# Kernel tuning notes

Hardware: AMD Instinct MI355X
Metric: run time of the kernel (lower is better)

Reference implementation:

```python
import jax, jax.numpy as jnp
import numpy as np

N = 20000      # nodes
E = 320000     # edges
IN = 128       # in_channels
HID = 64       # hidden_channels (per-head out dim, concat=False -> mean over heads)
HEADS = 4
NEG_SLOPE = 0.2


def setup_inputs() -> dict:
    key = jax.random.key(0)
    ks = jax.random.split(key, 18)
    g = lambda i, shape: jax.random.normal(ks[i], shape, dtype=jnp.float32) * 0.05
    return {
        "x": jax.random.normal(ks[0], (N, IN), dtype=jnp.float32),
        "edge_index": jax.random.randint(ks[1], (2, E), 0, N),
        # GATConv params: lin weight (no bias in PyG lin), att_src/att_dst, out bias
        "W0": g(2, (IN, HEADS * HID)),
        "W1": g(3, (HID, HEADS * HID)),
        "W2": g(4, (HID, HEADS * HID)),
        "W3": g(5, (HID, HEADS * HID)),
        "a_src": g(6, (4, HEADS, HID)),
        "a_dst": g(7, (4, HEADS, HID)),
        "gat_b": g(8, (4, HID)),
        # residual projection for layer 0 (in_channels != hidden_channels)
        "res_W": g(9, (IN, HID)),
        "res_b": g(10, (HID,)),
        # edge classifier MLP: 2*HID -> HID -> HID -> 1
        "lin_W0": g(11, (2 * HID, HID)),
        "lin_b0": g(12, (HID,)),
        "lin_W1": g(13, (HID, HID)),
        "lin_b1": g(14, (HID,)),
        "lin_W2": g(15, (HID, 1)),
        "lin_b2": g(16, (1,)),
    }


def gat_conv(x, src, dst, W, asrc, adst, b, n):
    # x: [n, F_in]; src/dst: [E_tot] (self-loops included); W: [F_in, H*C]
    h = (x @ W).reshape(n, HEADS, HID)                     # [n, H, C]
    s_src = (h * asrc).sum(-1)                             # [n, H]
    s_dst = (h * adst).sum(-1)                             # [n, H]
    e = jax.nn.leaky_relu(s_src[src] + s_dst[dst], NEG_SLOPE)  # [E_tot, H]
    # segment softmax over incoming edges of each dst node
    m = jax.ops.segment_max(e, dst, num_segments=n)        # [n, H]
    p = jnp.exp(e - m[dst])
    z = jax.ops.segment_sum(p, dst, num_segments=n)
    alpha = p / z[dst]                                     # [E_tot, H]
    out = jax.ops.segment_sum(alpha[:, :, None] * h[src], dst, num_segments=n)  # [n, H, C]
    return out.mean(axis=1) + b                            # concat=False -> mean over heads


def reference(x, edge_index, W0, W1, W2, W3, a_src, a_dst, gat_b,
              res_W, res_b, lin_W0, lin_b0, lin_W1, lin_b1, lin_W2, lin_b2):
    n = x.shape[0]
    loop = jnp.arange(n)
    src = jnp.concatenate([edge_index[0], loop])  # PyG GATConv adds self-loops
    dst = jnp.concatenate([edge_index[1], loop])
    Ws = [W0, W1, W2, W3]
    h = x
    for i in range(4):
        h_prev = h
        h = gat_conv(h, src, dst, Ws[i], a_src[i], a_dst[i], gat_b[i], n)
        if i == 0:
            h = h + h_prev @ res_W + res_b   # projected residual
        else:
            h = h + h_prev
        h = jax.nn.elu(h)
    row, col = edge_index[0], edge_index[1]
    er = jnp.concatenate([h[row], h[col]], axis=1)        # [E, 2*HID]
    er = jax.nn.relu(er @ lin_W0 + lin_b0)                # shapes differ -> no residual
    er = jax.nn.relu(er @ lin_W1 + lin_b1 + er)           # shapes match -> residual
    logits = er @ lin_W2 + lin_b2                          # [E, 1]
    return logits
```

## Files before the change

kernel.cpp:

```cpp
#include <hip/hip_runtime.h>
#include <hip/hip_bf16.h>

#define NSLOPE 0.2f
#define MAXDEG 64

typedef short bf16x8 __attribute__((ext_vector_type(8)));
typedef float f32x4 __attribute__((ext_vector_type(4)));

__device__ __forceinline__ unsigned short f2b(float f) {
    unsigned u = __float_as_uint(f);
    unsigned r = (u + 0x7FFFu + ((u >> 16) & 1u)) >> 16;
    return (unsigned short)r;
}
__device__ __forceinline__ float b2f_lo(unsigned w) {
    return __uint_as_float(w << 16);
}
__device__ __forceinline__ float b2f_hi(unsigned w) {
    return __uint_as_float(w & 0xFFFF0000u);
}
__device__ __forceinline__ float b2f_s(short s) {
    return __uint_as_float(((unsigned)(unsigned short)s) << 16);
}
__device__ __forceinline__ unsigned packb(float lo, float hi) {
    return ((unsigned)f2b(hi) << 16) | (unsigned)f2b(lo);
}

__global__ __launch_bounds__(256) void prep_all(
    const float* __restrict__ W0, const float* __restrict__ W1,
    const float* __restrict__ W2, const float* __restrict__ W3,
    const float* __restrict__ resW, const float* __restrict__ linW0,
    const float* __restrict__ linW1, const float* __restrict__ linB0,
    const float* __restrict__ a_src, const float* __restrict__ a_dst,
    const float* __restrict__ gat_b, const float* __restrict__ res_b,
    short* __restrict__ WtC0e, short* __restrict__ WtC1,
    short* __restrict__ WtC2, short* __restrict__ WtC3,
    short* __restrict__ WtUV, short* __restrict__ WbT,
    float* __restrict__ wsd0, float* __restrict__ wsdL,
    float* __restrict__ bias128, float* __restrict__ gb0res,
    int* __restrict__ deg, int n) {
    const int bx = blockIdx.x;
    const int tid = threadIdx.x;
    if (bx == 0) {
        for (int idx = blockIdx.y * 256 + tid; idx < 64 * 640; idx += 256 * 16) {
            int j = idx / 640, k = idx - j * 640;
            float v;
            if (k < 512) {
                int h = k >> 7, kk = k & 127;
                v = W0[kk * 256 + h * 64 + j];
            } else {
                v = resW[(k - 512) * 64 + j];
            }
            WtC0e[idx] = (short)f2b(v);
        }
    } else if (bx <= 3) {
        const float* src = (bx == 1) ? W1 : (bx == 2) ? W2 : W3;
        short* dst = (bx == 1) ? WtC1 : (bx == 2) ? WtC2 : WtC3;
        for (int idx = blockIdx.y * 256 + tid; idx < 64 * 256; idx += 256 * 16) {
            int j = idx >> 8, rem = idx & 255;
            int h = rem >> 6, kk = rem & 63;
            dst[idx] = (short)f2b(src[kk * 256 + h * 64 + j]);
        }
    } else if (bx == 4) {
        if (blockIdx.y) return;
        for (int idx = tid; idx < 64 * 64; idx += 256) {
            int nn = idx >> 6, k = idx & 63;
            WtUV[idx] = (short)f2b(linW0[k * 64 + nn]);
        }
    } else if (bx == 5) {
        if (blockIdx.y) return;
        for (int idx = tid; idx < 64 * 64; idx += 256) {
            int nn = idx >> 6, k = idx & 63;
            WtUV[64 * 64 + idx] = (short)f2b(linW0[(k + 64) * 64 + nn]);
        }
    } else if (bx == 6) {
        if (blockIdx.y) return;
        for (int idx = tid; idx < 64 * 64; idx += 256) {
            int nn = idx >> 6, k = idx & 63;
            WbT[idx] = (short)f2b(linW1[k * 64 + nn]);
        }
    } else if (bx == 7) {
        if (blockIdx.y) return;
        if (tid < 128)
            bias128[tid] = (tid < 64) ? linB0[tid] : 0.f;
        else if (tid < 192)
            gb0res[tid - 128] = gat_b[tid - 128] + res_b[tid - 128];
    } else if (bx <= 11) {
        if (blockIdx.y) return;
        int l = bx - 8;
        const float* W = (l == 0) ? W0 : (l == 1) ? W1 : (l == 2) ? W2 : W3;
        const int K = (l == 0) ? 128 : 64;
        float* dst = (l == 0) ? wsd0 : wsdL + (l - 1) * 64 * 8;
        for (int idx = tid; idx < K * 8; idx += 256) {
            int k = idx >> 3, j = idx & 7, h = j & 3;
            const float* av = ((j < 4) ? a_src : a_dst) + l * 256 + h * 64;
            const float* wr = W + k * 256 + h * 64;
            float s = 0.f;
#pragma unroll 8
            for (int c = 0; c < 64; ++c) s += wr[c] * av[c];
            dst[k * 8 + j] = s;
        }
    } else {
        for (int i = blockIdx.y * 256 + tid; i < n; i += 256 * 16) deg[i] = 0;
    }
}

__global__ __launch_bounds__(256) void fill_convert(
    const int* __restrict__ ei, int* __restrict__ deg, int* __restrict__ csrS,
    int E, const float* __restrict__ x, const float* __restrict__ wsd0,
    unsigned* __restrict__ xb2, float* __restrict__ Ssrc,
    float* __restrict__ Sdst, int n, int eBlocks) {
    if ((int)blockIdx.x < eBlocks) {
        int e = blockIdx.x * 256 + threadIdx.x;
        if (e >= E) return;
        int s = ei[e], d = ei[E + e];
        int pos = atomicAdd(&deg[d], 1);
        if (pos < MAXDEG) csrS[d * MAXDEG + pos] = s;
        return;
    }
    const int nb = blockIdx.x - eBlocks;
    const int wid = threadIdx.x >> 6;
    const int lane = threadIdx.x & 63;
    const int node = nb * 4 + wid;
    if (node >= n) return;
    float2 xv = *(const float2*)&x[(size_t)node * 128 + lane * 2];
    xb2[(size_t)node * 64 + lane] = packb(xv.x, xv.y);
    float pv[8];
    const float* w0 = &wsd0[(lane * 2) * 8];
    const float* w1 = &wsd0[(lane * 2 + 1) * 8];
#pragma unroll
    for (int j = 0; j < 8; ++j) pv[j] = xv.x * w0[j] + xv.y * w1[j];
#pragma unroll
    for (int off = 1; off < 64; off <<= 1) {
#pragma unroll
        for (int j = 0; j < 8; ++j) pv[j] += __shfl_xor(pv[j], off, 64);
    }
    if (lane == 0) {
        *(float4*)&Ssrc[node * 4] = make_float4(pv[0], pv[1], pv[2], pv[3]);
        *(float4*)&Sdst[node * 4] = make_float4(pv[4], pv[5], pv[6], pv[7]);
    }
}

__global__ __launch_bounds__(256) void gat_gather128(
    const int* __restrict__ csrS, const int* __restrict__ deg,
    const float* __restrict__ Ssrc, const float* __restrict__ Sdst,
    const unsigned* __restrict__ xin, unsigned* __restrict__ aggB, int n) {
    const int wid = threadIdx.x >> 6;
    const int lane = threadIdx.x & 63;
    const int node = blockIdx.x * 4 + wid;
    if (node >= n) return;
    const int dn = min(deg[node], MAXDEG);
    const int sreg = (lane < dn) ? csrS[node * MAXDEG + lane] : 0;
    const float4 sd = *(const float4*)&Sdst[node * 4];
    const float4 ss = *(const float4*)&Ssrc[node * 4];
    float c0 = ss.x + sd.x, c1 = ss.y + sd.y, c2 = ss.z + sd.z,
          c3 = ss.w + sd.w;
    c0 = c0 > 0.f ? c0 : NSLOPE * c0;
    c1 = c1 > 0.f ? c1 : NSLOPE * c1;
    c2 = c2 > 0.f ? c2 : NSLOPE * c2;
    c3 = c3 > 0.f ? c3 : NSLOPE * c3;
    float ps0 = __expf(c0), ps1 = __expf(c1), ps2 = __expf(c2),
          ps3 = __expf(c3);
    unsigned own = xin[(size_t)node * 64 + lane];
    float f0o = b2f_lo(own), f1o = b2f_hi(own);
    float u00 = ps0 * f0o, u01 = ps0 * f1o;
    float u10 = ps1 * f0o, u11 = ps1 * f1o;
    float u20 = ps2 * f0o, u21 = ps2 * f1o;
    float u30 = ps3 * f0o, u31 = ps3 * f1o;
    float z0 = ps0, z1 = ps1, z2 = ps2, z3 = ps3;
#pragma unroll 4
    for (int p = 0; p < dn; ++p) {
        int sj = __shfl(sreg, p, 64);
        float4 sv = *(const float4*)&Ssrc[sj * 4];
        unsigned fv = xin[(size_t)sj * 64 + lane];
        float e0 = sv.x + sd.x, e1 = sv.y + sd.y;
        float e2 = sv.z + sd.z, e3 = sv.w + sd.w;
        e0 = e0 > 0.f ? e0 : NSLOPE * e0;
        e1 = e1 > 0.f ? e1 : NSLOPE * e1;
        e2 = e2 > 0.f ? e2 : NSLOPE * e2;
        e3 = e3 > 0.f ? e3 : NSLOPE * e3;
        float p0 = __expf(e0), p1 = __expf(e1);
        float p2 = __expf(e2), p3 = __expf(e3);
        float f0 = b2f_lo(fv), f1 = b2f_hi(fv);
        u00 += p0 * f0; u01 += p0 * f1;
        u10 += p1 * f0; u11 += p1 * f1;
        u20 += p2 * f0; u21 += p2 * f1;
        u30 += p3 * f0; u31 += p3 * f1;
        z0 += p0; z1 += p1; z2 += p2; z3 += p3;
    }
    float i0 = 0.25f / z0, i1 = 0.25f / z1, i2 = 0.25f / z2, i3 = 0.25f / z3;
    size_t base = (size_t)node * 320;
    aggB[base + lane] = packb(u00 * i0, u01 * i0);
    aggB[base + 64 + lane] = packb(u10 * i1, u11 * i1);
    aggB[base + 128 + lane] = packb(u20 * i2, u21 * i2);
    aggB[base + 192 + lane] = packb(u30 * i3, u31 * i3);
    aggB[base + 256 + lane] = own;
}

__global__ __launch_bounds__(256) void gat_gather64(
    const int* __restrict__ csrS, const int* __restrict__ deg,
    const float* __restrict__ Ssrc, const float* __restrict__ Sdst,
    const unsigned* __restrict__ fin, unsigned* __restrict__ aggB, int n) {
    const int wid = threadIdx.x >> 6;
    const int lane = threadIdx.x & 63;
    const int half = lane >> 5;
    const int cl = lane & 31;
    const int node = blockIdx.x * 4 + wid;
    if (node >= n) return;
    const int dn = min(deg[node], MAXDEG);
    const int sreg = (lane < dn) ? csrS[node * MAXDEG + lane] : 0;
    const float4 sd = *(const float4*)&Sdst[node * 4];
    const float4 ss = *(const float4*)&Ssrc[node * 4];
    float c0 = ss.x + sd.x, c1 = ss.y + sd.y, c2 = ss.z + sd.z,
          c3 = ss.w + sd.w;
    c0 = c0 > 0.f ? c0 : NSLOPE * c0;
    c1 = c1 > 0.f ? c1 : NSLOPE * c1;
    c2 = c2 > 0.f ? c2 : NSLOPE * c2;
    c3 = c3 > 0.f ? c3 : NSLOPE * c3;
    float ps0 = __expf(c0), ps1 = __expf(c1), ps2 = __expf(c2),
          ps3 = __expf(c3);
    unsigned own = fin[(size_t)node * 32 + cl];
    float u00 = 0.f, u01 = 0.f, u10 = 0.f, u11 = 0.f;
    float u20 = 0.f, u21 = 0.f, u30 = 0.f, u31 = 0.f;
    float z0 = 0.f, z1 = 0.f, z2 = 0.f, z3 = 0.f;
#pragma unroll 4
    for (int p = half; p < dn; p += 2) {
        int sj = __shfl(sreg, p, 64);
        float4 sv = *(const float4*)&Ssrc[sj * 4];
        unsigned fv = fin[(size_t)sj * 32 + cl];
        float e0 = sv.x + sd.x, e1 = sv.y + sd.y;
        float e2 = sv.z + sd.z, e3 = sv.w + sd.w;
        e0 = e0 > 0.f ? e0 : NSLOPE * e0;
        e1 = e1 > 0.f ? e1 : NSLOPE * e1;
        e2 = e2 > 0.f ? e2 : NSLOPE * e2;
        e3 = e3 > 0.f ? e3 : NSLOPE * e3;
        float p0 = __expf(e0), p1 = __expf(e1);
        float p2 = __expf(e2), p3 = __expf(e3);
        float f0 = b2f_lo(fv), f1 = b2f_hi(fv);
        u00 += p0 * f0; u01 += p0 * f1;
        u10 += p1 * f0; u11 += p1 * f1;
        u20 += p2 * f0; u21 += p2 * f1;
        u30 += p3 * f0; u31 += p3 * f1;
        z0 += p0; z1 += p1; z2 += p2; z3 += p3;
    }
    u00 += __shfl_xor(u00, 32, 64); u01 += __shfl_xor(u01, 32, 64);
    u10 += __shfl_xor(u10, 32, 64); u11 += __shfl_xor(u11, 32, 64);
    u20 += __shfl_xor(u20, 32, 64); u21 += __shfl_xor(u21, 32, 64);
    u30 += __shfl_xor(u30, 32, 64); u31 += __shfl_xor(u31, 32, 64);
    z0 += __shfl_xor(z0, 32, 64); z1 += __shfl_xor(z1, 32, 64);
    z2 += __shfl_xor(z2, 32, 64); z3 += __shfl_xor(z3, 32, 64);
    if (half == 0) {
        float f0o = b2f_lo(own), f1o = b2f_hi(own);
        u00 += ps0 * f0o; u01 += ps0 * f1o;
        u10 += ps1 * f0o; u11 += ps1 * f1o;
        u20 += ps2 * f0o; u21 += ps2 * f1o;
        u30 += ps3 * f0o; u31 += ps3 * f1o;
        z0 += ps0; z1 += ps1; z2 += ps2; z3 += ps3;
        float i0 = 0.25f / z0, i1 = 0.25f / z1;
        float i2 = 0.25f / z2, i3 = 0.25f / z3;
        size_t base = (size_t)node * 128;
        aggB[base + cl] = packb(u00 * i0, u01 * i0);
        aggB[base + 32 + cl] = packb(u10 * i1, u11 * i1);
        aggB[base + 64 + cl] = packb(u20 * i2, u21 * i2);
        aggB[base + 96 + cl] = packb(u30 * i3, u31 * i3);
    }
}

template <int KK, bool SCORES>
__global__ __launch_bounds__(256) void gemm_layer(
    const short* __restrict__ Xb, const short* __restrict__ Wt,
    const float* __restrict__ gbias, const float* __restrict__ resid,
    const float* __restrict__ wsd, float* __restrict__ feat,
    short* __restrict__ featb, float* __restrict__ Ssrc,
    float* __restrict__ Sdst, int n) {
    __shared__ __align__(16) short Xs[64 * 136];
    __shared__ __align__(16) short Ws[64 * 40];
    const int tid = threadIdx.x;
    const int nb = blockIdx.x * 64;
    const int wid = tid >> 6;
    const int lane = tid & 63;
    const int t = lane & 15, quad = lane >> 4;
    f32x4 acc[4];
#pragma unroll
    for (int g = 0; g < 4; ++g) acc[g] = (f32x4){0.f, 0.f, 0.f, 0.f};
#pragma unroll 1
    for (int c0 = 0; c0 < KK / 128; ++c0) {
        __syncthreads();
        for (int idx = tid; idx < 1024; idx += 256) {
            int row = idx >> 4, c = idx & 15;
            uint4 v = make_uint4(0, 0, 0, 0);
            if (nb + row < n)
                v = *(const uint4*)(Xb + (size_t)(nb + row) * KK + c0 * 128 +
                                    c * 8);
            *(uint4*)(Xs + row * 136 + c * 8) = v;
        }
#pragma unroll 1
        for (int kc = 0; kc < 4; ++kc) {
            __syncthreads();
            {
                int row = tid >> 2, c = tid & 3;
                uint4 v = *(const uint4*)(Wt + (size_t)row * KK + c0 * 128 +
                                          kc * 32 + c * 8);
                *(uint4*)(Ws + row * 40 + c * 8) = v;
            }
            __syncthreads();
            bf16x8 a =
                *(const bf16x8*)(Xs + (wid * 16 + t) * 136 + kc * 32 + quad * 8);
#pragma unroll
            for (int g = 0; g < 4; ++g) {
                bf16x8 b = *(const bf16x8*)(Ws + (g * 16 + t) * 40 + quad * 8);
                acc[g] =
                    __builtin_amdgcn_mfma_f32_16x16x32_bf16(a, b, acc[g], 0, 0, 0);
            }
        }
    }
    float bv[4];
#pragma unroll
    for (int g = 0; g < 4; ++g) bv[g] = gbias[g * 16 + t];
    float wsv[4][8];
    if (SCORES) {
#pragma unroll
        for (int g = 0; g < 4; ++g) {
            float4 lo = *(const float4*)&wsd[(g * 16 + t) * 8];
            float4 hi = *(const float4*)&wsd[(g * 16 + t) * 8 + 4];
            wsv[g][0] = lo.x; wsv[g][1] = lo.y; wsv[g][2] = lo.z;
            wsv[g][3] = lo.w; wsv[g][4] = hi.x; wsv[g][5] = hi.y;
            wsv[g][6] = hi.z; wsv[g][7] = hi.w;
        }
    }
#pragma unroll
    for (int r = 0; r < 4; ++r) {
        int node = nb + wid * 16 + quad * 4 + r;
        bool ok = node < n;
        float val[4];
#pragma unroll
        for (int g = 0; g < 4; ++g) {
            float v = acc[g][r] + bv[g];
            if (resid && ok) v += resid[(size_t)node * 64 + g * 16 + t];
            v = v > 0.f ? v : expm1f(v);
            val[g] = v;
            if (ok) {
                feat[(size_t)node * 64 + g * 16 + t] = v;
                featb[(size_t)node * 64 + g * 16 + t] = (short)f2b(v);
            }
        }
        if (SCORES) {
            float pv[8];
#pragma unroll
            for (int j = 0; j < 8; ++j) {
                pv[j] = val[0] * wsv[0][j] + val[1] * wsv[1][j] +
                        val[2] * wsv[2][j] + val[3] * wsv[3][j];
            }
#pragma unroll
            for (int off = 1; off < 16; off <<= 1) {
#pragma unroll
                for (int j = 0; j < 8; ++j) pv[j] += __shfl_xor(pv[j], off, 64);
            }
            if (t == 0 && ok) {
                *(float4*)&Ssrc[node * 4] =
                    make_float4(pv[0], pv[1], pv[2], pv[3]);
                *(float4*)&Sdst[node * 4] =
                    make_float4(pv[4], pv[5], pv[6], pv[7]);
            }
        }
    }
}

__global__ __launch_bounds__(256) void gemm_layer_uv(
    const short* __restrict__ Xb, const short* __restrict__ Wt,
    const float* __restrict__ gbias, const float* __restrict__ resid,
    const short* __restrict__ WtUV, const float* __restrict__ bias128,
    short* __restrict__ OutUV, int n) {
    constexpr int KK = 256;
    __shared__ __align__(16) short Xs[64 * 136];
    __shared__ __align__(16) short Ws[128 * 40];
    const int tid = threadIdx.x;
    const int nb = blockIdx.x * 64;
    const int wid = tid >> 6;
    const int lane = tid & 63;
    const int t = lane & 15, quad = lane >> 4;
    f32x4 acc[4];
#pragma unroll
    for (int g = 0; g < 4; ++g) acc[g] = (f32x4){0.f, 0.f, 0.f, 0.f};
#pragma unroll 1
    for (int c0 = 0; c0 < KK / 128; ++c0) {
        __syncthreads();
        for (int idx = tid; idx < 1024; idx += 256) {
            int row = idx >> 4, c = idx & 15;
            uint4 v = make_uint4(0, 0, 0, 0);
            if (nb + row < n)
                v = *(const uint4*)(Xb + (size_t)(nb + row) * KK + c0 * 128 +
                                    c * 8);
            *(uint4*)(Xs + row * 136 + c * 8) = v;
        }
#pragma unroll 1
        for (int kc = 0; kc < 4; ++kc) {
            __syncthreads();
            {
                int row = tid >> 2, c = tid & 3;
                uint4 v = *(const uint4*)(Wt + (size_t)row * KK + c0 * 128 +
                                          kc * 32 + c * 8);
                *(uint4*)(Ws + row * 40 + c * 8) = v;
            }
            __syncthreads();
            bf16x8 a =
                *(const bf16x8*)(Xs + (wid * 16 + t) * 136 + kc * 32 + quad * 8);
#pragma unroll
            for (int g = 0; g < 4; ++g) {
                bf16x8 b = *(const bf16x8*)(Ws + (g * 16 + t) * 40 + quad * 8);
                acc[g] =
                    __builtin_amdgcn_mfma_f32_16x16x32_bf16(a, b, acc[g], 0, 0, 0);
            }
        }
    }
    float bv[4];
#pragma unroll
    for (int g = 0; g < 4; ++g) bv[g] = gbias[g * 16 + t];
    __syncthreads();
#pragma unroll
    for (int r = 0; r < 4; ++r) {
        int node = nb + wid * 16 + quad * 4 + r;
        bool ok = node < n;
        int lrow = wid * 16 + quad * 4 + r;
#pragma unroll
        for (int g = 0; g < 4; ++g) {
            float v = acc[g][r] + bv[g];
            if (ok) v += resid[(size_t)node * 64 + g * 16 + t];
            v = v > 0.f ? v : expm1f(v);
            Xs[lrow * 72 + g * 16 + t] = (short)f2b(v);
        }
    }
    f32x4 acc2[8];
#pragma unroll
    for (int g = 0; g < 8; ++g) acc2[g] = (f32x4){0.f, 0.f, 0.f, 0.f};
#pragma unroll 1
    for (int kc = 0; kc < 2; ++kc) {
        __syncthreads();
        for (int idx = tid; idx < 512; idx += 256) {
            int row = idx >> 2, c = idx & 3;
            uint4 v = *(const uint4*)(WtUV + (size_t)row * 64 + kc * 32 + c * 8);
            *(uint4*)(Ws + row * 40 + c * 8) = v;
        }
        __syncthreads();
        bf16x8 a = *(const bf16x8*)(Xs + (wid * 16 + t) * 72 + kc * 32 + quad * 8);
#pragma unroll
        for (int g = 0; g < 8; ++g) {
            bf16x8 b = *(const bf16x8*)(Ws + (g * 16 + t) * 40 + quad * 8);
            acc2[g] = __builtin_amdgcn_mfma_f32_16x16x32_bf16(a, b, acc2[g], 0, 0, 0);
        }
    }
    float b2[8];
#pragma unroll
    for (int g = 0; g < 8; ++g) b2[g] = bias128[g * 16 + t];
#pragma unroll
    for (int r = 0; r < 4; ++r) {
        int node = nb + wid * 16 + quad * 4 + r;
        if (node >= n) continue;
#pragma unroll
        for (int g = 0; g < 8; ++g)
            OutUV[(size_t)node * 128 + g * 16 + t] =
                (short)f2b(acc2[g][r] + b2[g]);
    }
}

__global__ __launch_bounds__(256) void edge_mlp3(
    const int* __restrict__ ei, const unsigned* __restrict__ UV,
    const short* __restrict__ WbT, const float* __restrict__ bb,
    const float* __restrict__ Wc, const float* __restrict__ bc,
    float* __restrict__ out, int E) {
    __shared__ __align__(16) short t1b[64 * 72];
    __shared__ __align__(16) short wbs[64 * 72];
    const int tid = threadIdx.x;
    const int eBase = blockIdx.x * 64;
    for (int idx = tid; idx < 512; idx += 256) {
        int row = idx >> 3, c = idx & 7;
        *(uint4*)(wbs + row * 72 + c * 8) =
            *(const uint4*)(WbT + row * 64 + c * 8);
    }
    {
        const int j = tid & 31;
        const int eg = tid >> 5;
        int rr[8], cc[8];
#pragma unroll
        for (int it = 0; it < 8; ++it) {
            int e = eBase + it * 8 + eg;
            rr[it] = (e < E) ? ei[e] : 0;
            cc[it] = (e < E) ? ei[E + e] : 0;
        }
#pragma unroll
        for (int it = 0; it < 8; ++it) {
            unsigned uu = UV[(size_t)rr[it] * 64 + j];
            unsigned vv = UV[(size_t)cc[it] * 64 + 32 + j];
            float lo = fmaxf(b2f_lo(uu) + b2f_lo(vv), 0.f);
            float hi = fmaxf(b2f_hi(uu) + b2f_hi(vv), 0.f);
            *(unsigned*)(t1b + (it * 8 + eg) * 72 + j * 2) = packb(lo, hi);
        }
    }
    __syncthreads();
    const int w = tid >> 6, lane = tid & 63;
    const int t = lane & 15, quad = lane >> 4;
    f32x4 acc[4];
#pragma unroll
    for (int g = 0; g < 4; ++g) acc[g] = (f32x4){0.f, 0.f, 0.f, 0.f};
#pragma unroll
    for (int kc = 0; kc < 2; ++kc) {
        bf16x8 a = *(const bf16x8*)(t1b + (w * 16 + t) * 72 + kc * 32 + quad * 8);
#pragma unroll
        for (int g = 0; g < 4; ++g) {
            bf16x8 b = *(const bf16x8*)(wbs + (g * 16 + t) * 72 + kc * 32 + quad * 8);
            acc[g] = __builtin_amdgcn_mfma_f32_16x16x32_bf16(a, b, acc[g], 0, 0, 0);
        }
    }
    float wcv[4], bbv[4];
#pragma unroll
    for (int g = 0; g < 4; ++g) {
        wcv[g] = Wc[g * 16 + t];
        bbv[g] = bb[g * 16 + t];
    }
    const float bcv = bc[0];
#pragma unroll
    for (int r = 0; r < 4; ++r) {
        int el = w * 16 + quad * 4 + r;
        float part = 0.f;
#pragma unroll
        for (int g = 0; g < 4; ++g) {
            float t1v = b2f_s(t1b[el * 72 + g * 16 + t]);
            float t2 = fmaxf(acc[g][r] + bbv[g] + t1v, 0.f);
            part += t2 * wcv[g];
        }
        part += __shfl_xor(part, 1, 64);
        part += __shfl_xor(part, 2, 64);
        part += __shfl_xor(part, 4, 64);
        part += __shfl_xor(part, 8, 64);
        int e = eBase + el;
        if (t == 0 && e < E) out[e] = part + bcv;
    }
}

extern "C" void kernel_launch(void* const* d_in, const int* in_sizes, int n_in,
                              void* d_out, int out_size, void* d_ws,
                              size_t ws_size, hipStream_t stream) {
    const float* x = (const float*)d_in[0];
    const int* ei = (const int*)d_in[1];
    const float* W0 = (const float*)d_in[2];
    const float* W1 = (const float*)d_in[3];
    const float* W2 = (const float*)d_in[4];
    const float* W3 = (const float*)d_in[5];
    const float* a_src = (const float*)d_in[6];
    const float* a_dst = (const float*)d_in[7];
    const float* gat_b = (const float*)d_in[8];
    const float* res_W = (const float*)d_in[9];
    const float* res_b = (const float*)d_in[10];
    const float* lin_W0 = (const float*)d_in[11];
    const float* lin_b0 = (const float*)d_in[12];
    const float* lin_W1 = (const float*)d_in[13];
    const float* lin_b1 = (const float*)d_in[14];
    const float* lin_W2 = (const float*)d_in[15];
    const float* lin_b2 = (const float*)d_in[16];
    float* out = (float*)d_out;

    const int N = in_sizes[0] / 128;
    const int E = in_sizes[1] / 2;

    char* ws = (char*)d_ws;
    unsigned* aggB = (unsigned*)ws;
    float* featA = (float*)(aggB + (size_t)N * 320);
    float* featB = featA + (size_t)N * 64;
    unsigned* xb2 = (unsigned*)(featB + (size_t)N * 64);
    unsigned* featbA = xb2 + (size_t)N * 64;
    unsigned* featbB = featbA + (size_t)N * 32;
    unsigned* UVb = featbB + (size_t)N * 32;
    float* Ssrc = (float*)(UVb + (size_t)N * 64);
    float* Sdst = Ssrc + (size_t)N * 4;
    short* WtC0e = (short*)(Sdst + (size_t)N * 4);
    short* WtC1 = WtC0e + 64 * 640;
    short* WtC2 = WtC1 + 64 * 256;
    short* WtC3 = WtC2 + 64 * 256;
    short* WtUV = WtC3 + 64 * 256;
    short* WbT = WtUV + 128 * 64;
    float* wsd0 = (float*)(WbT + 64 * 64);
    float* wsdL = wsd0 + 128 * 8;
    float* bias128 = wsdL + 3 * 64 * 8;
    float* gb0res = bias128 + 128;
    int* deg = (int*)(gb0res + 64);
    int* csrS = deg + N;

    const int gemmBlocks = (N + 63) / 64;
    const int eBlocks = (E + 255) / 256;
    const int nodeW = (N + 3) / 4;

    prep_all<<<dim3(13, 16), 256, 0, stream>>>(
        W0, W1, W2, W3, res_W, lin_W0, lin_W1, lin_b0, a_src, a_dst, gat_b,
        res_b, WtC0e, WtC1, WtC2, WtC3, WtUV, WbT, wsd0, wsdL, bias128,
        gb0res, deg, N);
    fill_convert<<<eBlocks + nodeW, 256, 0, stream>>>(
        ei, deg, csrS, E, x, wsd0, xb2, Ssrc, Sdst, N, eBlocks);

    gat_gather128<<<nodeW, 256, 0, stream>>>(csrS, deg, Ssrc, Sdst, xb2, aggB,
                                             N);
    gemm_layer<640, true><<<gemmBlocks, 256, 0, stream>>>(
        (const short*)aggB, WtC0e, gb0res, nullptr, wsdL, featA,
        (short*)featbA, Ssrc, Sdst, N);

    gat_gather64<<<nodeW, 256, 0, stream>>>(csrS, deg, Ssrc, Sdst, featbA,
                                            aggB, N);
    gemm_layer<256, true><<<gemmBlocks, 256, 0, stream>>>(
        (const short*)aggB, WtC1, gat_b + 64, featA, wsdL + 64 * 8, featB,
        (short*)featbB, Ssrc, Sdst, N);
    gat_gather64<<<nodeW, 256, 0, stream>>>(csrS, deg, Ssrc, Sdst, featbB,
                                            aggB, N);
    gemm_layer<256, true><<<gemmBlocks, 256, 0, stream>>>(
        (const short*)aggB, WtC2, gat_b + 128, featB, wsdL + 2 * 64 * 8,
        featA, (short*)featbA, Ssrc, Sdst, N);

    gat_gather64<<<nodeW, 256, 0, stream>>>(csrS, deg, Ssrc, Sdst, featbA,
                                            aggB, N);
    gemm_layer_uv<<<gemmBlocks, 256, 0, stream>>>(
        (const short*)aggB, WtC3, gat_b + 192, featA, WtUV, bias128,
        (short*)UVb, N);

    edge_mlp3<<<(E + 63) / 64, 256, 0, stream>>>(ei, UVb, WbT, lin_b1, lin_W2,
                                                 lin_b2, out, E);
}
```

Baseline: 327.7 us.

## Fuse neighbor gather with layer GEMM for GAT layers 1-3

Replaces the separate gather kernel and GEMM kernel for layers 1-3 with one 512-thread kernel. Each block gathers attention-weighted neighbor aggregates for 64 nodes straight into shared memory, then runs the MFMA GEMM with 8 waves split over rows and column halves. This removes the aggB round trip through global memory and half the launches. Attention scores are now double-buffered (SsrcB/SdstB) so one block's writes do not race with other blocks still reading the previous layer's scores. The risk is lower parallelism in the gather phase (one block per 64 nodes) and a __syncthreads inside the per-row score-reduction loop.

```diff
diff --git a/kernel.cpp b/kernel.cpp
--- a/kernel.cpp
+++ b/kernel.cpp
@@ -196,75 +196,6 @@
     aggB[base + 256 + lane] = own;
 }
 
-__global__ __launch_bounds__(256) void gat_gather64(
-    const int* __restrict__ csrS, const int* __restrict__ deg,
-    const float* __restrict__ Ssrc, const float* __restrict__ Sdst,
-    const unsigned* __restrict__ fin, unsigned* __restrict__ aggB, int n) {
-    const int wid = threadIdx.x >> 6;
-    const int lane = threadIdx.x & 63;
-    const int half = lane >> 5;
-    const int cl = lane & 31;
-    const int node = blockIdx.x * 4 + wid;
-    if (node >= n) return;
-    const int dn = min(deg[node], MAXDEG);
-    const int sreg = (lane < dn) ? csrS[node * MAXDEG + lane] : 0;
-    const float4 sd = *(const float4*)&Sdst[node * 4];
-    const float4 ss = *(const float4*)&Ssrc[node * 4];
-    float c0 = ss.x + sd.x, c1 = ss.y + sd.y, c2 = ss.z + sd.z,
-          c3 = ss.w + sd.w;
-    c0 = c0 > 0.f ? c0 : NSLOPE * c0;
-    c1 = c1 > 0.f ? c1 : NSLOPE * c1;
-    c2 = c2 > 0.f ? c2 : NSLOPE * c2;
-    c3 = c3 > 0.f ? c3 : NSLOPE * c3;
-    float ps0 = __expf(c0), ps1 = __expf(c1), ps2 = __expf(c2),
-          ps3 = __expf(c3);
-    unsigned own = fin[(size_t)node * 32 + cl];
-    float u00 = 0.f, u01 = 0.f, u10 = 0.f, u11 = 0.f;
-    float u20 = 0.f, u21 = 0.f, u30 = 0.f, u31 = 0.f;
-    float z0 = 0.f, z1 = 0.f, z2 = 0.f, z3 = 0.f;
-#pragma unroll 4
-    for (int p = half; p < dn; p += 2) {
-        int sj = __shfl(sreg, p, 64);
-        float4 sv = *(const float4*)&Ssrc[sj * 4];
-        unsigned fv = fin[(size_t)sj * 32 + cl];
-        float e0 = sv.x + sd.x, e1 = sv.y + sd.y;
-        float e2 = sv.z + sd.z, e3 = sv.w + sd.w;
-        e0 = e0 > 0.f ? e0 : NSLOPE * e0;
-        e1 = e1 > 0.f ? e1 : NSLOPE * e1;
-        e2 = e2 > 0.f ? e2 : NSLOPE * e2;
-        e3 = e3 > 0.f ? e3 : NSLOPE * e3;
-        float p0 = __expf(e0), p1 = __expf(e1);
-        float p2 = __expf(e2), p3 = __expf(e3);
-        float f0 = b2f_lo(fv), f1 = b2f_hi(fv);
-        u00 += p0 * f0; u01 += p0 * f1;
-        u10 += p1 * f0; u11 += p1 * f1;
-        u20 += p2 * f0; u21 += p2 * f1;
-        u30 += p3 * f0; u31 += p3 * f1;
-        z0 += p0; z1 += p1; z2 += p2; z3 += p3;
-    }
-    u00 += __shfl_xor(u00, 32, 64); u01 += __shfl_xor(u01, 32, 64);
-    u10 += __shfl_xor(u10, 32, 64); u11 += __shfl_xor(u11, 32, 64);
-    u20 += __shfl_xor(u20, 32, 64); u21 += __shfl_xor(u21, 32, 64);
-    u30 += __shfl_xor(u30, 32, 64); u31 += __shfl_xor(u31, 32, 64);
-    z0 += __shfl_xor(z0, 32, 64); z1 += __shfl_xor(z1, 32, 64);
-    z2 += __shfl_xor(z2, 32, 64); z3 += __shfl_xor(z3, 32, 64);
-    if (half == 0) {
-        float f0o = b2f_lo(own), f1o = b2f_hi(own);
-        u00 += ps0 * f0o; u01 += ps0 * f1o;
-        u10 += ps1 * f0o; u11 += ps1 * f1o;
-        u20 += ps2 * f0o; u21 += ps2 * f1o;
-        u30 += ps3 * f0o; u31 += ps3 * f1o;
-        z0 += ps0; z1 += ps1; z2 += ps2; z3 += ps3;
-        float i0 = 0.25f / z0, i1 = 0.25f / z1;
-        float i2 = 0.25f / z2, i3 = 0.25f / z3;
-        size_t base = (size_t)node * 128;
-        aggB[base + cl] = packb(u00 * i0, u01 * i0);
-        aggB[base + 32 + cl] = packb(u10 * i1, u11 * i1);
-        aggB[base + 64 + cl] = packb(u20 * i2, u21 * i2);
-        aggB[base + 96 + cl] = packb(u30 * i3, u31 * i3);
-    }
-}
-
 template <int KK, bool SCORES>
 __global__ __launch_bounds__(256) void gemm_layer(
     const short* __restrict__ Xb, const short* __restrict__ Wt,
@@ -365,100 +296,221 @@
     }
 }
 
-__global__ __launch_bounds__(256) void gemm_layer_uv(
-    const short* __restrict__ Xb, const short* __restrict__ Wt,
+template <bool UV>
+__global__ __launch_bounds__(512) void fused_layer(
+    const int* __restrict__ csrS, const int* __restrict__ deg,
+    const float* __restrict__ Sin_s, const float* __restrict__ Sin_d,
+    const unsigned* __restrict__ fin, const short* __restrict__ Wt,
     const float* __restrict__ gbias, const float* __restrict__ resid,
-    const short* __restrict__ WtUV, const float* __restrict__ bias128,
-    short* __restrict__ OutUV, int n) {
-    constexpr int KK = 256;
-    __shared__ __align__(16) short Xs[64 * 136];
-    __shared__ __align__(16) short Ws[128 * 40];
+    const float* __restrict__ wsd, float* __restrict__ feat,
+    short* __restrict__ featb, float* __restrict__ Sout_s,
+    float* __restrict__ Sout_d, const short* __restrict__ WtUV,
+    const float* __restrict__ bias128, short* __restrict__ OutUV, int n) {
+    __shared__ __align__(16) short Xs[64 * 272];
+    __shared__ __align__(16) float Sred[64][8];
     const int tid = threadIdx.x;
     const int nb = blockIdx.x * 64;
     const int wid = tid >> 6;
     const int lane = tid & 63;
+    const int half = lane >> 5;
+    const int cl = lane & 31;
+#pragma unroll 1
+    for (int i = 0; i < 8; ++i) {
+        const int r = wid * 8 + i;
+        const int node = nb + r;
+        if (node >= n) {
+            if (half == 0) {
+                int base = r * 272 + 2 * cl;
+                *(unsigned*)(Xs + base) = 0u;
+                *(unsigned*)(Xs + base + 64) = 0u;
+                *(unsigned*)(Xs + base + 136) = 0u;
+                *(unsigned*)(Xs + base + 200) = 0u;
+            }
+            continue;
+        }
+        const int dn = min(deg[node], MAXDEG);
+        const int sreg = (lane < dn) ? csrS[node * MAXDEG + lane] : 0;
+        const float4 sd = *(const float4*)&Sin_d[node * 4];
+        const float4 ss = *(const float4*)&Sin_s[node * 4];
+        float sc0 = ss.x + sd.x, sc1 = ss.y + sd.y;
+        float sc2 = ss.z + sd.z, sc3 = ss.w + sd.w;
+        sc0 = sc0 > 0.f ? sc0 : NSLOPE * sc0;
+        sc1 = sc1 > 0.f ? sc1 : NSLOPE * sc1;
+        sc2 = sc2 > 0.f ? sc2 : NSLOPE * sc2;
+        sc3 = sc3 > 0.f ? sc3 : NSLOPE * sc3;
+        float ps0 = __expf(sc0), ps1 = __expf(sc1);
+        float ps2 = __expf(sc2), ps3 = __expf(sc3);
+        unsigned own = fin[(size_t)node * 32 + cl];
+        float u00 = 0.f, u01 = 0.f, u10 = 0.f, u11 = 0.f;
+        float u20 = 0.f, u21 = 0.f, u30 = 0.f, u31 = 0.f;
+        float z0 = 0.f, z1 = 0.f, z2 = 0.f, z3 = 0.f;
+#pragma unroll 4
+        for (int p = half; p < dn; p += 2) {
+            int sj = __shfl(sreg, p, 64);
+            float4 sv = *(const float4*)&Sin_s[sj * 4];
+            unsigned fv = fin[(size_t)sj * 32 + cl];
+            float e0 = sv.x + sd.x, e1 = sv.y + sd.y;
+            float e2 = sv.z + sd.z, e3 = sv.w + sd.w;
+            e0 = e0 > 0.f ? e0 : NSLOPE * e0;
+            e1 = e1 > 0.f ? e1 : NSLOPE * e1;
+            e2 = e2 > 0.f ? e2 : NSLOPE * e2;
+            e3 = e3 > 0.f ? e3 : NSLOPE * e3;
+            float p0 = __expf(e0), p1 = __expf(e1);
+            float p2 = __expf(e2), p3 = __expf(e3);
+            float f0 = b2f_lo(fv), f1 = b2f_hi(fv);
+            u00 += p0 * f0; u01 += p0 * f1;
+            u10 += p1 * f0; u11 += p1 * f1;
+            u20 += p2 * f0; u21 += p2 * f1;
+            u30 += p3 * f0; u31 += p3 * f1;
+            z0 += p0; z1 += p1; z2 += p2; z3 += p3;
+        }
+        u00 += __shfl_xor(u00, 32, 64); u01 += __shfl_xor(u01, 32, 64);
+        u10 += __shfl_xor(u10, 32, 64); u11 += __shfl_xor(u11, 32, 64);
+        u20 += __shfl_xor(u20, 32, 64); u21 += __shfl_xor(u21, 32, 64);
+        u30 += __shfl_xor(u30, 32, 64); u31 += __shfl_xor(u31, 32, 64);
+        z0 += __shfl_xor(z0, 32, 64); z1 += __shfl_xor(z1, 32, 64);
+        z2 += __shfl_xor(z2, 32, 64); z3 += __shfl_xor(z3, 32, 64);
+        if (half == 0) {
+            float f0o = b2f_lo(own), f1o = b2f_hi(own);
+            u00 += ps0 * f0o; u01 += ps0 * f1o;
+            u10 += ps1 * f0o; u11 += ps1 * f1o;
+            u20 += ps2 * f0o; u21 += ps2 * f1o;
+            u30 += ps3 * f0o; u31 += ps3 * f1o;
+            z0 += ps0; z1 += ps1; z2 += ps2; z3 += ps3;
+            float i0 = 0.25f / z0, i1 = 0.25f / z1;
+            float i2 = 0.25f / z2, i3 = 0.25f / z3;
+            int base = r * 272 + 2 * cl;
+            *(unsigned*)(Xs + base) = packb(u00 * i0, u01 * i0);
+            *(unsigned*)(Xs + base + 64) = packb(u10 * i1, u11 * i1);
+            *(unsigned*)(Xs + base + 136) = packb(u20 * i2, u21 * i2);
+            *(unsigned*)(Xs + base + 200) = packb(u30 * i3, u31 * i3);
+        }
+    }
+    __syncthreads();
+    const int wrow = wid & 3;
+    const int wcol = wid >> 2;
     const int t = lane & 15, quad = lane >> 4;
-    f32x4 acc[4];
-#pragma unroll
-    for (int g = 0; g < 4; ++g) acc[g] = (f32x4){0.f, 0.f, 0.f, 0.f};
-#pragma unroll 1
-    for (int c0 = 0; c0 < KK / 128; ++c0) {
+    f32x4 acc[2];
+    acc[0] = (f32x4){0.f, 0.f, 0.f, 0.f};
+    acc[1] = (f32x4){0.f, 0.f, 0.f, 0.f};
+#pragma unroll
+    for (int ch = 0; ch < 2; ++ch) {
+#pragma unroll
+        for (int kc = 0; kc < 4; ++kc) {
+            bf16x8 a = *(const bf16x8*)(Xs + (wrow * 16 + t) * 272 + ch * 136 +
+                                        kc * 32 + quad * 8);
+#pragma unroll
+            for (int g = 0; g < 2; ++g) {
+                bf16x8 b = *(const bf16x8*)(Wt +
+                                            (size_t)(wcol * 32 + g * 16 + t) *
+                                                256 +
+                                            ch * 128 + kc * 32 + quad * 8);
+                acc[g] = __builtin_amdgcn_mfma_f32_16x16x32_bf16(a, b, acc[g],
+                                                                 0, 0, 0);
+            }
+        }
+    }
+    float bv[2];
+#pragma unroll
+    for (int g = 0; g < 2; ++g) bv[g] = gbias[wcol * 32 + g * 16 + t];
+    if constexpr (!UV) {
+        float wsv[2][8];
+#pragma unroll
+        for (int g = 0; g < 2; ++g) {
+            float4 lo = *(const float4*)&wsd[((wcol * 2 + g) * 16 + t) * 8];
+            float4 hi = *(const float4*)&wsd[((wcol * 2 + g) * 16 + t) * 8 + 4];
+            wsv[g][0] = lo.x; wsv[g][1] = lo.y; wsv[g][2] = lo.z;
+            wsv[g][3] = lo.w; wsv[g][4] = hi.x; wsv[g][5] = hi.y;
+            wsv[g][6] = hi.z; wsv[g][7] = hi.w;
+        }
+#pragma unroll
+        for (int r = 0; r < 4; ++r) {
+            const int row = wrow * 16 + quad * 4 + r;
+            const int node = nb + row;
+            const bool ok = node < n;
+            float val[2];
+#pragma unroll
+            for (int g = 0; g < 2; ++g) {
+                float v = acc[g][r] + bv[g];
+                if (ok) v += resid[(size_t)node * 64 + wcol * 32 + g * 16 + t];
+                v = v > 0.f ? v : expm1f(v);
+                val[g] = v;
+                if (ok) {
+                    feat[(size_t)node * 64 + wcol * 32 + g * 16 + t] = v;
+                    featb[(size_t)node * 64 + wcol * 32 + g * 16 + t] =
+                        (short)f2b(v);
+                }
+            }
+            float pv[8];
+#pragma unroll
+            for (int j = 0; j < 8; ++j)
+                pv[j] = val[0] * wsv[0][j] + val[1] * wsv[1][j];
+#pragma unroll
+            for (int off = 1; off < 16; off <<= 1) {
+#pragma unroll
+                for (int j = 0; j < 8; ++j) pv[j] += __shfl_xor(pv[j], off, 64);
+            }
+            if (wcol == 1 && t == 0) {
+                *(float4*)&Sred[row][0] =
+                    make_float4(pv[0], pv[1], pv[2], pv[3]);
+                *(float4*)&Sred[row][4] =
+                    make_float4(pv[4], pv[5], pv[6], pv[7]);
+            }
+            __syncthreads();
+            if (wcol == 0 && t == 0 && ok) {
+                float4 o0 = *(const float4*)&Sred[row][0];
+                float4 o1 = *(const float4*)&Sred[row][4];
+                *(float4*)&Sout_s[node * 4] = make_float4(
+                    pv[0] + o0.x, pv[1] + o0.y, pv[2] + o0.z, pv[3] + o0.w);
+                *(float4*)&Sout_d[node * 4] = make_float4(
+                    pv[4] + o1.x, pv[5] + o1.y, pv[6] + o1.z, pv[7] + o1.w);
+            }
+        }
+    } else {
         __syncthreads();
-        for (int idx = tid; idx < 1024; idx += 256) {
-            int row = idx >> 4, c = idx & 15;
-            uint4 v = make_uint4(0, 0, 0, 0);
-            if (nb + row < n)
-                v = *(const uint4*)(Xb + (size_t)(nb + row) * KK + c0 * 128 +
-                                    c * 8);
-            *(uint4*)(Xs + row * 136 + c * 8) = v;
-        }
-#pragma unroll 1
-        for (int kc = 0; kc < 4; ++kc) {
-            __syncthreads();
-            {
-                int row = tid >> 2, c = tid & 3;
-                uint4 v = *(const uint4*)(Wt + (size_t)row * KK + c0 * 128 +
-                                          kc * 32 + c * 8);
-                *(uint4*)(Ws + row * 40 + c * 8) = v;
-            }
-            __syncthreads();
-            bf16x8 a =
-                *(const bf16x8*)(Xs + (wid * 16 + t) * 136 + kc * 32 + quad * 8);
+#pragma unroll
+        for (int r = 0; r < 4; ++r) {
+            const int row = wrow * 16 + quad * 4 + r;
+            const int node = nb + row;
+            const bool ok = node < n;
+#pragma unroll
+            for (int g = 0; g < 2; ++g) {
+                float v = acc[g][r] + bv[g];
+                if (ok) v += resid[(size_t)node * 64 + wcol * 32 + g * 16 + t];
+                v = v > 0.f ? v : expm1f(v);
+                Xs[row * 72 + wcol * 32 + g * 16 + t] = (short)f2b(v);
+            }
+        }
+        __syncthreads();
+        f32x4 acc2[4];
+#pragma unroll
+        for (int g = 0; g < 4; ++g) acc2[g] = (f32x4){0.f, 0.f, 0.f, 0.f};
+#pragma unroll
+        for (int kc = 0; kc < 2; ++kc) {
+            bf16x8 a = *(const bf16x8*)(Xs + (wrow * 16 + t) * 72 + kc * 32 +
+                                        quad * 8);
 #pragma unroll
             for (int g = 0; g < 4; ++g) {
-                bf16x8 b = *(const bf16x8*)(Ws + (g * 16 + t) * 40 + quad * 8);
-                acc[g] =
-                    __builtin_amdgcn_mfma_f32_16x16x32_bf16(a, b, acc[g], 0, 0, 0);
-            }
-        }
-    }
-    float bv[4];
-#pragma unroll
-    for (int g = 0; g < 4; ++g) bv[g] = gbias[g * 16 + t];
-    __syncthreads();
-#pragma unroll
-    for (int r = 0; r < 4; ++r) {
-        int node = nb + wid * 16 + quad * 4 + r;
-        bool ok = node < n;
-        int lrow = wid * 16 + quad * 4 + r;
-#pragma unroll
-        for (int g = 0; g < 4; ++g) {
-            float v = acc[g][r] + bv[g];
-            if (ok) v += resid[(size_t)node * 64 + g * 16 + t];
-            v = v > 0.f ? v : expm1f(v);
-            Xs[lrow * 72 + g * 16 + t] = (short)f2b(v);
-        }
-    }
-    f32x4 acc2[8];
-#pragma unroll
-    for (int g = 0; g < 8; ++g) acc2[g] = (f32x4){0.f, 0.f, 0.f, 0.f};
-#pragma unroll 1
-    for (int kc = 0; kc < 2; ++kc) {
-        __syncthreads();
-        for (int idx = tid; idx < 512; idx += 256) {
-            int row = idx >> 2, c = idx & 3;
-            uint4 v = *(const uint4*)(WtUV + (size_t)row * 64 + kc * 32 + c * 8);
-            *(uint4*)(Ws + row * 40 + c * 8) = v;
-        }
-        __syncthreads();
-        bf16x8 a = *(const bf16x8*)(Xs + (wid * 16 + t) * 72 + kc * 32 + quad * 8);
-#pragma unroll
-        for (int g = 0; g < 8; ++g) {
-            bf16x8 b = *(const bf16x8*)(Ws + (g * 16 + t) * 40 + quad * 8);
-            acc2[g] = __builtin_amdgcn_mfma_f32_16x16x32_bf16(a, b, acc2[g], 0, 0, 0);
-        }
-    }
-    float b2[8];
-#pragma unroll
-    for (int g = 0; g < 8; ++g) b2[g] = bias128[g * 16 + t];
-#pragma unroll
-    for (int r = 0; r < 4; ++r) {
-        int node = nb + wid * 16 + quad * 4 + r;
-        if (node >= n) continue;
-#pragma unroll
-        for (int g = 0; g < 8; ++g)
-            OutUV[(size_t)node * 128 + g * 16 + t] =
-                (short)f2b(acc2[g][r] + b2[g]);
+                bf16x8 b = *(const bf16x8*)(WtUV +
+                                            (size_t)(wcol * 64 + g * 16 + t) *
+                                                64 +
+                                            kc * 32 + quad * 8);
+                acc2[g] = __builtin_amdgcn_mfma_f32_16x16x32_bf16(a, b, acc2[g],
+                                                                  0, 0, 0);
+            }
+        }
+        float b2[4];
+#pragma unroll
+        for (int g = 0; g < 4; ++g) b2[g] = bias128[wcol * 64 + g * 16 + t];
+#pragma unroll
+        for (int r = 0; r < 4; ++r) {
+            const int node = nb + wrow * 16 + quad * 4 + r;
+            if (node >= n) continue;
+#pragma unroll
+            for (int g = 0; g < 4; ++g)
+                OutUV[(size_t)node * 128 + wcol * 64 + g * 16 + t] =
+                    (short)f2b(acc2[g][r] + b2[g]);
+        }
     }
 }
 
@@ -571,7 +623,9 @@
     unsigned* UVb = featbB + (size_t)N * 32;
     float* Ssrc = (float*)(UVb + (size_t)N * 64);
     float* Sdst = Ssrc + (size_t)N * 4;
-    short* WtC0e = (short*)(Sdst + (size_t)N * 4);
+    float* SsrcB = Sdst + (size_t)N * 4;
+    float* SdstB = SsrcB + (size_t)N * 4;
+    short* WtC0e = (short*)(SdstB + (size_t)N * 4);
     short* WtC1 = WtC0e + 64 * 640;
     short* WtC2 = WtC1 + 64 * 256;
     short* WtC3 = WtC2 + 64 * 256;
@@ -601,22 +655,18 @@
         (const short*)aggB, WtC0e, gb0res, nullptr, wsdL, featA,
         (short*)featbA, Ssrc, Sdst, N);
 
-    gat_gather64<<<nodeW, 256, 0, stream>>>(csrS, deg, Ssrc, Sdst, featbA,
-                                            aggB, N);
-    gemm_layer<256, true><<<gemmBlocks, 256, 0, stream>>>(
-        (const short*)aggB, WtC1, gat_b + 64, featA, wsdL + 64 * 8, featB,
-        (short*)featbB, Ssrc, Sdst, N);
-    gat_gather64<<<nodeW, 256, 0, stream>>>(csrS, deg, Ssrc, Sdst, featbB,
-                                            aggB, N);
-    gemm_layer<256, true><<<gemmBlocks, 256, 0, stream>>>(
-        (const short*)aggB, WtC2, gat_b + 128, featB, wsdL + 2 * 64 * 8,
-        featA, (short*)featbA, Ssrc, Sdst, N);
-
-    gat_gather64<<<nodeW, 256, 0, stream>>>(csrS, deg, Ssrc, Sdst, featbA,
-                                            aggB, N);
-    gemm_layer_uv<<<gemmBlocks, 256, 0, stream>>>(
-        (const short*)aggB, WtC3, gat_b + 192, featA, WtUV, bias128,
-        (short*)UVb, N);
+    fused_layer<false><<<gemmBlocks, 512, 0, stream>>>(
+        csrS, deg, Ssrc, Sdst, featbA, WtC1, gat_b + 64, featA,
+        wsdL + 64 * 8, featB, (short*)featbB, SsrcB, SdstB, nullptr, nullptr,
+        nullptr, N);
+    fused_layer<false><<<gemmBlocks, 512, 0, stream>>>(
+        csrS, deg, SsrcB, SdstB, featbB, WtC2, gat_b + 128, featB,
+        wsdL + 2 * 64 * 8, featA, (short*)featbA, Ssrc, Sdst, nullptr,
+        nullptr, nullptr, N);
+
+    fused_layer<true><<<gemmBlocks, 512, 0, stream>>>(
+        csrS, deg, Ssrc, Sdst, featbA, WtC3, gat_b + 192, featA, nullptr,
+        nullptr, nullptr, nullptr, nullptr, WtUV, bias128, (short*)UVb, N);
 
     edge_mlp3<<<(E + 63) / 64, 256, 0, stream>>>(ei, UVb, WbT, lin_b1, lin_W2,
                                                  lin_b2, out, E);
```

After: 394.4 us. +20.4%, slower.
